# Performance work log

Measured on AMD Instinct MI355X. Metric: run time of the kernel, lower is better.

The kernel has to match this reference:

```python
import math
import jax, jax.numpy as jnp
import numpy as np

B, S, D = 4, 2048, 1024
EPS_LN = 1e-5
EPS_MAS = 1e-9


def layernorm(x, g, b):
    m = jnp.mean(x, axis=-1, keepdims=True)
    v = jnp.mean(jnp.square(x - m), axis=-1, keepdims=True)
    return (x - m) * jax.lax.rsqrt(v + EPS_LN) * g + b


def spl(x, proto_w, mu_w, mu_b, gate):
    # match_values = x @ proto^T / sqrt(d);  comp = silu(x @ mu^T + b)
    match = jnp.einsum('bsd,od->bso', x, proto_w) / math.sqrt(x.shape[-1])
    comp = jax.nn.silu(jnp.einsum('bsd,od->bso', x, mu_w) + mu_b)
    return comp, match, gate


def branch(comp, match, gate, passthrough):
    # mas_normalize on the 1-D gate vector (cost), broadcast over [B,S,D]
    cost = gate / (jnp.max(jnp.abs(gate)) + EPS_MAS)
    rl = match - cost
    mrl = jax.nn.relu(rl)
    mask = (rl > 0).astype(comp.dtype)
    return comp * mrl + passthrough * (1.0 - mask)


def causal_attention(q, k, v):
    # num_heads = 1, head_dim = D, is_causal=True
    scale = 1.0 / math.sqrt(q.shape[-1])
    scores = jnp.einsum('bqd,bkd->bqk', q, k) * scale
    causal = jnp.tril(jnp.ones((q.shape[1], k.shape[1]), dtype=bool))
    scores = jnp.where(causal, scores, jnp.asarray(-1e9, scores.dtype))
    p = jax.nn.softmax(scores, axis=-1)
    return jnp.einsum('bqk,bkd->bqd', p, v)


def setup_inputs() -> dict:
    key = jax.random.key(0)
    ks = jax.random.split(key, 16)
    d = D
    std = 0.02
    inp = {
        'x': jax.random.normal(ks[0], (B, S, d), jnp.float32),
        'ln_g': jnp.ones((d,), jnp.float32),
        'ln_b': jnp.zeros((d,), jnp.float32),
    }
    names = ['q', 'k', 'v', 'o']
    for i, n in enumerate(names):
        inp[f'{n}_mu_w'] = std * jax.random.normal(ks[1 + 3 * i], (d, d), jnp.float32)
        inp[f'{n}_mu_b'] = jnp.zeros((d,), jnp.float32)
        inp[f'{n}_proto'] = std * jax.random.normal(ks[2 + 3 * i], (d, d), jnp.float32)
        inp[f'{n}_gate'] = 0.1 * jax.random.normal(ks[3 + 3 * i], (d,), jnp.float32)
    return inp


def reference(x, ln_g, ln_b,
              q_mu_w, q_mu_b, q_proto, q_gate,
              k_mu_w, k_mu_b, k_proto, k_gate,
              v_mu_w, v_mu_b, v_proto, v_gate,
              o_mu_w, o_mu_b, o_proto, o_gate):
    ln1_out = layernorm(x, ln_g, ln_b)

    c_q, mv_q, g_q = spl(ln1_out, q_proto, q_mu_w, q_mu_b, q_gate)
    c_k, mv_k, g_k = spl(ln1_out, k_proto, k_mu_w, k_mu_b, k_gate)
    c_v, mv_v, g_v = spl(ln1_out, v_proto, v_mu_w, v_mu_b, v_gate)

    q = branch(c_q, mv_q, g_q, ln1_out)
    k = branch(c_k, mv_k, g_k, ln1_out)
    v = branch(c_v, mv_v, g_v, ln1_out)

    attn_out = causal_attention(q, k, v)

    c_o, mv_o, g_o = spl(attn_out, o_proto, o_mu_w, o_mu_b, o_gate)
    masked_o = branch(c_o, mv_o, g_o, attn_out)

    x_out = x + masked_o
    return x_out
```

## Files before the change

### kernel.cpp

```cpp
#include <hip/hip_runtime.h>
#include <hip/hip_bf16.h>
#include <cmath>
#include <cstdint>

typedef _Float16 f16;
typedef _Float16 f16x8 __attribute__((ext_vector_type(8)));
typedef float f32x4 __attribute__((ext_vector_type(4)));

#define D_ 1024
#define S_ 2048


__device__ __forceinline__ void gload_lds16(const void* g, void* l) {
  __builtin_amdgcn_global_load_lds(
      (const __attribute__((address_space(1))) void*)(unsigned long long)(uintptr_t)g,
      (__attribute__((address_space(3))) void*)(unsigned int)(uintptr_t)l,
      16, 0, 0);
}

__device__ __forceinline__ int lds_off(int row, int cb) {
  return (row << 5) + ((cb ^ ((row >> 1) & 3)) << 3);
}

__device__ __forceinline__ void split1024(float v, f16& h, f16& l) {
  float s = v * 1024.f;
  h = (f16)s;
  l = (f16)(s - (float)h);
}

#define MFMA16(a, b, c) __builtin_amdgcn_mfma_f32_16x16x32_f16((a), (b), (c), 0, 0, 0)

__global__ __launch_bounds__(256) void convert_w(
    const float* __restrict__ s0, const float* __restrict__ s1,
    const float* __restrict__ s2, const float* __restrict__ s3,
    const float* __restrict__ s4, const float* __restrict__ s5,
    const float* __restrict__ s6, const float* __restrict__ s7,
    f16* __restrict__ dst) {
  const float* srcs[8] = {s0, s1, s2, s3, s4, s5, s6, s7};
  const float* sp = srcs[blockIdx.y];
  f16* hi = dst + (size_t)blockIdx.y * 2097152;
  f16* lo = hi + 1048576;
  const int i = (blockIdx.x * 256 + threadIdx.x) << 2;
  float4 f = *(const float4*)(sp + i);
  __align__(8) f16 h4[4], l4[4];
  split1024(f.x, h4[0], l4[0]); split1024(f.y, h4[1], l4[1]);
  split1024(f.z, h4[2], l4[2]); split1024(f.w, h4[3], l4[3]);
  *(uint2*)(hi + i) = *(uint2*)h4;
  *(uint2*)(lo + i) = *(uint2*)l4;
}

__global__ __launch_bounds__(256) void cost_k(
    const float* __restrict__ g0, const float* __restrict__ g1,
    const float* __restrict__ g2, const float* __restrict__ g3,
    float* __restrict__ cost) {
  const float* gp = blockIdx.x == 0 ? g0 : blockIdx.x == 1 ? g1
                   : blockIdx.x == 2 ? g2 : g3;
  const int t = threadIdx.x;
  float4 v = *(const float4*)(gp + (t << 2));
  float mx = fmaxf(fmaxf(fabsf(v.x), fabsf(v.y)), fmaxf(fabsf(v.z), fabsf(v.w)));
  for (int o = 32; o; o >>= 1) mx = fmaxf(mx, __shfl_xor(mx, o, 64));
  __shared__ float red[4];
  if ((t & 63) == 0) red[t >> 6] = mx;
  __syncthreads();
  mx = fmaxf(fmaxf(red[0], red[1]), fmaxf(red[2], red[3]));
  const float den = mx + 1e-9f;
  float4 o = {v.x / den, v.y / den, v.z / den, v.w / den};
  *(float4*)(cost + (blockIdx.x << 10) + (t << 2)) = o;
}

__global__ __launch_bounds__(256) void layernorm_k(
    const float* __restrict__ x, const float* __restrict__ g,
    const float* __restrict__ bta, f16* __restrict__ Lh, f16* __restrict__ Ll) {
  const int row = blockIdx.x, t = threadIdx.x;
  const float* xr = x + (size_t)row * D_;
  float4 v = *(const float4*)(xr + (t << 2));
  float s = v.x + v.y + v.z + v.w;
  float q = v.x * v.x + v.y * v.y + v.z * v.z + v.w * v.w;
  for (int o = 32; o; o >>= 1) { s += __shfl_xor(s, o, 64); q += __shfl_xor(q, o, 64); }
  __shared__ float red[8];
  const int wid = t >> 6;
  if ((t & 63) == 0) { red[wid] = s; red[4 + wid] = q; }
  __syncthreads();
  s = red[0] + red[1] + red[2] + red[3];
  q = red[4] + red[5] + red[6] + red[7];
  const float mean = s * (1.f / D_);
  const float var = q * (1.f / D_) - mean * mean;
  const float inv = 1.f / sqrtf(var + 1e-5f);
  float4 gv = *(const float4*)(g + (t << 2));
  float4 bv = *(const float4*)(bta + (t << 2));
  __align__(8) f16 h4[4], l4[4];
  split1024((v.x - mean) * inv * gv.x + bv.x, h4[0], l4[0]);
  split1024((v.y - mean) * inv * gv.y + bv.y, h4[1], l4[1]);
  split1024((v.z - mean) * inv * gv.z + bv.z, h4[2], l4[2]);
  split1024((v.w - mean) * inv * gv.w + bv.w, h4[3], l4[3]);
  const size_t off = (size_t)row * D_ + (t << 2);
  *(uint2*)(Lh + off) = *(uint2*)h4;
  *(uint2*)(Ll + off) = *(uint2*)l4;
}

template <int EPI, int MUP>
__global__ __launch_bounds__(1024) void dual_gemm_v5(
    const f16* __restrict__ Ah, const f16* __restrict__ Al,
    const f16* __restrict__ Wph, const f16* __restrict__ Wpl,
    const f16* __restrict__ Wmh, const f16* __restrict__ Wml,
    const float* __restrict__ bias, const float* __restrict__ cost,
    const f16* __restrict__ passh, const f16* __restrict__ passl,
    const float* __restrict__ xres, f16* __restrict__ outh,
    f16* __restrict__ outl, float* __restrict__ outf) {
  __shared__ __align__(16) f16 smem[65536];
  const int tid = threadIdx.x, wid = tid >> 6, lane = tid & 63;
  const int row0 = blockIdx.x << 8, col0 = blockIdx.y << 7;
  const int wr = (wid & 3) << 6;
  const int wc = (wid >> 2) << 5;
  const int arow = lane & 15, cbk = lane >> 4;

  const int srow = tid >> 2;
  const int scA = ((tid & 3) ^ ((srow >> 1) & 3)) << 3;
  const int wrow = srow & 127;
  const int scW = ((tid & 3) ^ ((wrow >> 1) & 3)) << 3;
  const int wsel = tid >> 9;
  const int dstA = wid << 9;
  const int dstW = 16384 + (wid << 9);
  const int dstW2 = 24576 + (wid << 9);

  const f16* pAh = Ah + (size_t)(row0 + srow) * D_ + scA;
  const f16* pAl = Al + (size_t)(row0 + srow) * D_ + scA;
  const f16* pW1 = (wsel ? Wpl : Wph) + (size_t)(col0 + wrow) * D_ + scW;
  const f16* pW2 = (wsel ? Wml : Wmh) + (size_t)(col0 + wrow) * D_ + scW;

  const f32x4 zero = {0.f, 0.f, 0.f, 0.f};
  f32x4 accP[4][2], accM[4][2];
#pragma unroll
  for (int m = 0; m < 4; ++m)
#pragma unroll
    for (int n = 0; n < 2; ++n) { accP[m][n] = zero; accM[m][n] = zero; }

  int aoff[4], boff[2];
#pragma unroll
  for (int m = 0; m < 4; ++m) aoff[m] = lds_off(wr + m * 16 + arow, cbk);
#pragma unroll
  for (int n = 0; n < 2; ++n) boff[n] = lds_off(wc + n * 16 + arow, cbk);

  gload_lds16(pAh, smem + dstA);
  gload_lds16(pAl, smem + 8192 + dstA);
  gload_lds16(pW1, smem + dstW);
  gload_lds16(pW2, smem + dstW2);

  int cur = 0;
  for (int t = 0; t < 32; ++t) {
    const f16* bb = smem + (cur << 15);
    f16* nb = smem + ((cur ^ 1) << 15);
    const int kn = (t < 31) ? ((t + 1) << 5) : 0;

    gload_lds16(pAh + kn, nb + dstA);
    gload_lds16(pAl + kn, nb + 8192 + dstA);
    gload_lds16(pW1 + kn, nb + dstW);
    gload_lds16(pW2 + kn, nb + dstW2);
    asm volatile("s_waitcnt vmcnt(4)\n\ts_barrier" ::: "memory");
    __builtin_amdgcn_sched_barrier(0);

    f16x8 ah[4], al[4];
#pragma unroll
    for (int m = 0; m < 4; ++m) {
      ah[m] = *(const f16x8*)&bb[aoff[m]];
      al[m] = *(const f16x8*)&bb[8192 + aoff[m]];
    }
    __builtin_amdgcn_s_setprio(1);
#pragma unroll
    for (int n = 0; n < 2; ++n) {
      const f16x8 bph = *(const f16x8*)&bb[16384 + boff[n]];
      const f16x8 bpl = *(const f16x8*)&bb[20480 + boff[n]];
      const f16x8 bmh = *(const f16x8*)&bb[24576 + boff[n]];
      const f16x8 bml = *(const f16x8*)&bb[28672 + boff[n]];
#pragma unroll
      for (int m = 0; m < 4; ++m) {
        accP[m][n] = MFMA16(ah[m], bph, accP[m][n]);
        accP[m][n] = MFMA16(ah[m], bpl, accP[m][n]);
        accP[m][n] = MFMA16(al[m], bph, accP[m][n]);
        accM[m][n] = MFMA16(ah[m], bmh, accM[m][n]);
        accM[m][n] = MFMA16(ah[m], bml, accM[m][n]);
        if (MUP == 3) accM[m][n] = MFMA16(al[m], bmh, accM[m][n]);
      }
    }
    __builtin_amdgcn_s_setprio(0);
    asm volatile("s_waitcnt lgkmcnt(0)\n\ts_barrier" ::: "memory");
    cur ^= 1;
  }

#pragma unroll
  for (int m = 0; m < 4; ++m) {
    const int rb = row0 + wr + m * 16 + ((lane >> 4) << 2);
#pragma unroll
    for (int n = 0; n < 2; ++n) {
      const int col = col0 + wc + n * 16 + (lane & 15);
      const float cb2 = cost[col], bbv = bias[col];
#pragma unroll
      for (int j = 0; j < 4; ++j) {
        const size_t off = (size_t)(rb + j) * D_ + col;
        const float match = accP[m][n][j] * (1.f / 33554432.f);
        const float pre = accM[m][n][j] * (1.f / 1048576.f) + bbv;
        const float comp = pre / (1.f + expf(-pre));
        const float rl = match - cb2;
        float ov;
        if (rl > 0.f) ov = comp * rl;
        else ov = ((float)passh[off] + (float)passl[off]) * (1.f / 1024.f);
        if (EPI == 0) {
          f16 h, l; split1024(ov, h, l);
          outh[off] = h; outl[off] = l;
        } else {
          outf[off] = xres[off] + ov;
        }
      }
    }
  }
}

__global__ __launch_bounds__(256) void transpose_v(
    const f16* __restrict__ Vh, const f16* __restrict__ Vl,
    f16* __restrict__ VTh, f16* __restrict__ VTl) {
  const int iz = blockIdx.z, b = iz & 3;
  const f16* src = (iz >> 2) ? Vl : Vh;
  f16* dst = (iz >> 2) ? VTl : VTh;
  const int d0 = blockIdx.x << 6, s0 = blockIdx.y << 6;
  __shared__ f16 tl[64][65];
  const int c = threadIdx.x & 63, r4 = threadIdx.x >> 6;
  const f16* vb = src + (size_t)b * S_ * D_;
#pragma unroll
  for (int i = 0; i < 16; ++i) {
    const int sr = (r4 << 4) + i;
    tl[sr][c] = vb[(size_t)(s0 + sr) * D_ + d0 + c];
  }
  __syncthreads();
  f16* db = dst + (size_t)b * D_ * S_;
#pragma unroll
  for (int i = 0; i < 16; ++i) {
    const int dr = (r4 << 4) + i;
    db[(size_t)(d0 + dr) * S_ + s0 + c] = tl[c][dr];
  }
}

__global__ __launch_bounds__(512) void scores_v5(
    const f16* __restrict__ Qh, const f16* __restrict__ Ql,
    const f16* __restrict__ Kh, const f16* __restrict__ Kl,
    float* __restrict__ SC) {
  const int rt = blockIdx.x, ct = blockIdx.y, b = blockIdx.z;
  if (ct > rt) return;
  __shared__ __align__(16) f16 smem[32768];
  const int tid = threadIdx.x, wid = tid >> 6, lane = tid & 63;
  const int row0 = rt << 7, col0 = ct << 7;
  const int wr = (wid & 1) << 6;
  const int wc = (wid >> 1) << 5;
  const int arow = lane & 15, cbk = lane >> 4;

  const int srow = tid >> 2;
  const int sc4 = ((tid & 3) ^ ((srow >> 1) & 3)) << 3;
  const int dstb = wid << 9;

  const f16* pQh = Qh + ((size_t)b * S_ + row0 + srow) * D_ + sc4;
  const f16* pQl = Ql + ((size_t)b * S_ + row0 + srow) * D_ + sc4;
  const f16* pKh = Kh + ((size_t)b * S_ + col0 + srow) * D_ + sc4;
  const f16* pKl = Kl + ((size_t)b * S_ + col0 + srow) * D_ + sc4;

  const f32x4 zero = {0.f, 0.f, 0.f, 0.f};
  f32x4 acc[4][2];
#pragma unroll
  for (int m = 0; m < 4; ++m)
#pragma unroll
    for (int n = 0; n < 2; ++n) acc[m][n] = zero;

  int aoff[4], boff[2];
#pragma unroll
  for (int m = 0; m < 4; ++m) aoff[m] = lds_off(wr + m * 16 + arow, cbk);
#pragma unroll
  for (int n = 0; n < 2; ++n) boff[n] = lds_off(wc + n * 16 + arow, cbk);

  gload_lds16(pQh, smem + dstb);
  gload_lds16(pQl, smem + 4096 + dstb);
  gload_lds16(pKh, smem + 8192 + dstb);
  gload_lds16(pKl, smem + 12288 + dstb);

  int cur = 0;
  for (int t = 0; t < 32; ++t) {
    const f16* bb = smem + (cur << 14);
    f16* nb = smem + ((cur ^ 1) << 14);
    const int kn = (t < 31) ? ((t + 1) << 5) : 0;

    gload_lds16(pQh + kn, nb + dstb);
    gload_lds16(pQl + kn, nb + 4096 + dstb);
    gload_lds16(pKh + kn, nb + 8192 + dstb);
    gload_lds16(pKl + kn, nb + 12288 + dstb);
    asm volatile("s_waitcnt vmcnt(4)\n\ts_barrier" ::: "memory");
    __builtin_amdgcn_sched_barrier(0);

    f16x8 ah[4], al[4];
#pragma unroll
    for (int m = 0; m < 4; ++m) {
      ah[m] = *(const f16x8*)&bb[aoff[m]];
      al[m] = *(const f16x8*)&bb[4096 + aoff[m]];
    }
    __builtin_amdgcn_s_setprio(1);
#pragma unroll
    for (int n = 0; n < 2; ++n) {
      const f16x8 bh = *(const f16x8*)&bb[8192 + boff[n]];
      const f16x8 bl = *(const f16x8*)&bb[12288 + boff[n]];
#pragma unroll
      for (int m = 0; m < 4; ++m) {
        acc[m][n] = MFMA16(ah[m], bh, acc[m][n]);
        acc[m][n] = MFMA16(ah[m], bl, acc[m][n]);
        acc[m][n] = MFMA16(al[m], bh, acc[m][n]);
      }
    }
    __builtin_amdgcn_s_setprio(0);
    asm volatile("s_waitcnt lgkmcnt(0)\n\ts_barrier" ::: "memory");
    cur ^= 1;
  }

  float* scb = SC + (size_t)b * S_ * S_;
#pragma unroll
  for (int m = 0; m < 4; ++m) {
    const int rb = row0 + wr + m * 16 + ((lane >> 4) << 2);
#pragma unroll
    for (int n = 0; n < 2; ++n) {
      const int col = col0 + wc + n * 16 + (lane & 15);
#pragma unroll
      for (int j = 0; j < 4; ++j)
        scb[(size_t)(rb + j) * S_ + col] = acc[m][n][j] * (1.f / 33554432.f);
    }
  }
}

__global__ __launch_bounds__(256) void softmax_rows(float* __restrict__ SC) {
  const int r = blockIdx.x;
  const int s = r & 2047;
  float* rowf = SC + (size_t)r * S_;
  const int t = threadIdx.x, c0 = t << 3;
  float f[8];
  float4 u0 = *(const float4*)(rowf + c0);
  float4 u1 = *(const float4*)(rowf + c0 + 4);
  f[0] = u0.x; f[1] = u0.y; f[2] = u0.z; f[3] = u0.w;
  f[4] = u1.x; f[5] = u1.y; f[6] = u1.z; f[7] = u1.w;
  float mx = -3.0e38f;
#pragma unroll
  for (int j = 0; j < 8; ++j)
    if (c0 + j <= s) mx = fmaxf(mx, f[j]);
  for (int o = 32; o; o >>= 1) mx = fmaxf(mx, __shfl_xor(mx, o, 64));
  __shared__ float red[8];
  const int wid = t >> 6;
  if ((t & 63) == 0) red[wid] = mx;
  __syncthreads();
  mx = fmaxf(fmaxf(red[0], red[1]), fmaxf(red[2], red[3]));
  float e[8];
  float sum = 0.f;
#pragma unroll
  for (int j = 0; j < 8; ++j) {
    e[j] = (c0 + j <= s) ? expf(f[j] - mx) : 0.f;
    sum += e[j];
  }
  for (int o = 32; o; o >>= 1) sum += __shfl_xor(sum, o, 64);
  if ((t & 63) == 0) red[4 + wid] = sum;
  __syncthreads();
  sum = red[4] + red[5] + red[6] + red[7];
  f16* rowh = (f16*)rowf;
  __align__(16) f16 ph[8], pl[8];
#pragma unroll
  for (int j = 0; j < 8; ++j) {
    float p = (e[j] / sum) * 2048.f;
    ph[j] = (f16)p;
    pl[j] = (f16)(p - (float)ph[j]);
  }
  *(uint4*)(rowh + c0) = *(uint4*)ph;
  *(uint4*)(rowh + 2048 + c0) = *(uint4*)pl;
}

__global__ __launch_bounds__(512) void pv_v5(
    const f16* __restrict__ P, const f16* __restrict__ VTh,
    const f16* __restrict__ VTl, f16* __restrict__ Ath, f16* __restrict__ Atl) {
  const int rt = blockIdx.x, ct = blockIdx.y, b = blockIdx.z;
  __shared__ __align__(16) f16 smem[32768];
  const int tid = threadIdx.x, wid = tid >> 6, lane = tid & 63;
  const int row0 = rt << 7, col0 = ct << 7;
  const int wr = (wid & 1) << 6;
  const int wc = (wid >> 1) << 5;
  const int arow = lane & 15, cbk = lane >> 4;

  const int srow = tid >> 2;
  const int sc4 = ((tid & 3) ^ ((srow >> 1) & 3)) << 3;
  const int dstb = wid << 9;

  const f16* pPh = P + ((size_t)b * S_ + row0 + srow) * 4096 + sc4;
  const f16* pPl = pPh + 2048;
  const f16* pVh = VTh + (size_t)b * D_ * S_ + (size_t)(col0 + srow) * S_ + sc4;
  const f16* pVl = VTl + (size_t)b * D_ * S_ + (size_t)(col0 + srow) * S_ + sc4;

  const f32x4 zero = {0.f, 0.f, 0.f, 0.f};
  f32x4 acc[4][2];
#pragma unroll
  for (int m = 0; m < 4; ++m)
#pragma unroll
    for (int n = 0; n < 2; ++n) acc[m][n] = zero;

  int aoff[4], boff[2];
#pragma unroll
  for (int m = 0; m < 4; ++m) aoff[m] = lds_off(wr + m * 16 + arow, cbk);
#pragma unroll
  for (int n = 0; n < 2; ++n) boff[n] = lds_off(wc + n * 16 + arow, cbk);

  const int steps = (rt + 1) << 2;

  gload_lds16(pPh, smem + dstb);
  gload_lds16(pPl, smem + 4096 + dstb);
  gload_lds16(pVh, smem + 8192 + dstb);
  gload_lds16(pVl, smem + 12288 + dstb);

  int cur = 0;
  for (int t = 0; t < steps; ++t) {
    const f16* bb = smem + (cur << 14);
    f16* nb = smem + ((cur ^ 1) << 14);
    const int kn = (t < steps - 1) ? ((t + 1) << 5) : 0;

    gload_lds16(pPh + kn, nb + dstb);
    gload_lds16(pPl + kn, nb + 4096 + dstb);
    gload_lds16(pVh + kn, nb + 8192 + dstb);
    gload_lds16(pVl + kn, nb + 12288 + dstb);
    asm volatile("s_waitcnt vmcnt(4)\n\ts_barrier" ::: "memory");
    __builtin_amdgcn_sched_barrier(0);

    f16x8 ah[4], al[4];
#pragma unroll
    for (int m = 0; m < 4; ++m) {
      ah[m] = *(const f16x8*)&bb[aoff[m]];
      al[m] = *(const f16x8*)&bb[4096 + aoff[m]];
    }
    __builtin_amdgcn_s_setprio(1);
#pragma unroll
    for (int n = 0; n < 2; ++n) {
      const f16x8 bh = *(const f16x8*)&bb[8192 + boff[n]];
      const f16x8 bl = *(const f16x8*)&bb[12288 + boff[n]];
#pragma unroll
      for (int m = 0; m < 4; ++m) {
        acc[m][n] = MFMA16(ah[m], bh, acc[m][n]);
        acc[m][n] = MFMA16(ah[m], bl, acc[m][n]);
        acc[m][n] = MFMA16(al[m], bh, acc[m][n]);
      }
    }
    __builtin_amdgcn_s_setprio(0);
    asm volatile("s_waitcnt lgkmcnt(0)\n\ts_barrier" ::: "memory");
    cur ^= 1;
  }

#pragma unroll
  for (int m = 0; m < 4; ++m) {
    const int rb = row0 + wr + m * 16 + ((lane >> 4) << 2);
#pragma unroll
    for (int n = 0; n < 2; ++n) {
      const int col = col0 + wc + n * 16 + (lane & 15);
#pragma unroll
      for (int j = 0; j < 4; ++j) {
        const float at = acc[m][n][j] * (1.f / 2097152.f);
        const size_t off = ((size_t)b * S_ + rb + j) * D_ + col;
        f16 h, l; split1024(at, h, l);
        Ath[off] = h; Atl[off] = l;
      }
    }
  }
}

extern "C" void kernel_launch(void* const* d_in, const int* in_sizes, int n_in,
                              void* d_out, int out_size, void* d_ws, size_t ws_size,
                              hipStream_t stream) {
  (void)in_sizes; (void)n_in; (void)out_size; (void)ws_size;
  const float* x      = (const float*)d_in[0];
  const float* ln_g   = (const float*)d_in[1];
  const float* ln_b   = (const float*)d_in[2];
  const float* q_mu_w = (const float*)d_in[3];
  const float* q_mu_b = (const float*)d_in[4];
  const float* q_pro  = (const float*)d_in[5];
  const float* q_gate = (const float*)d_in[6];
  const float* k_mu_w = (const float*)d_in[7];
  const float* k_mu_b = (const float*)d_in[8];
  const float* k_pro  = (const float*)d_in[9];
  const float* k_gate = (const float*)d_in[10];
  const float* v_mu_w = (const float*)d_in[11];
  const float* v_mu_b = (const float*)d_in[12];
  const float* v_pro  = (const float*)d_in[13];
  const float* v_gate = (const float*)d_in[14];
  const float* o_mu_w = (const float*)d_in[15];
  const float* o_mu_b = (const float*)d_in[16];
  const float* o_pro  = (const float*)d_in[17];
  const float* o_gate = (const float*)d_in[18];

  char* w = (char*)d_ws;
  f16* WB = (f16*)w;
  const size_t WS = 2097152;
  f16* Lh  = (f16*)(w + 33554432);
  f16* Ll  = (f16*)(w + 50331648);
  f16* Qh  = (f16*)(w + 67108864);
  f16* Ql  = (f16*)(w + 83886080);
  f16* Kh  = (f16*)(w + 100663296);
  f16* Kl  = (f16*)(w + 117440512);
  f16* VTh = (f16*)(w + 134217728);
  f16* VTl = (f16*)(w + 150994944);
  float* SC = (float*)(w + 167772160);
  float* COST = (float*)(w + 234881024);
  f16* Vh = (f16*)SC;
  f16* Vl = (f16*)(w + 184549376);
  f16* Ath = Qh;  f16* Atl = Ql;

  convert_w<<<dim3(1024, 8), 256, 0, stream>>>(
      q_pro, q_mu_w, k_pro, k_mu_w, v_pro, v_mu_w, o_pro, o_mu_w, WB);
  cost_k<<<4, 256, 0, stream>>>(q_gate, k_gate, v_gate, o_gate, COST);
  layernorm_k<<<8192, 256, 0, stream>>>(x, ln_g, ln_b, Lh, Ll);

  dual_gemm_v5<0, 3><<<dim3(32, 8), 1024, 0, stream>>>(
      Lh, Ll, WB, WB + 1048576, WB + WS, WB + WS + 1048576,
      q_mu_b, COST, Lh, Ll, nullptr, Qh, Ql, nullptr);
  dual_gemm_v5<0, 3><<<dim3(32, 8), 1024, 0, stream>>>(
      Lh, Ll, WB + 2 * WS, WB + 2 * WS + 1048576, WB + 3 * WS, WB + 3 * WS + 1048576,
      k_mu_b, COST + 1024, Lh, Ll, nullptr, Kh, Kl, nullptr);
  dual_gemm_v5<0, 3><<<dim3(32, 8), 1024, 0, stream>>>(
      Lh, Ll, WB + 4 * WS, WB + 4 * WS + 1048576, WB + 5 * WS, WB + 5 * WS + 1048576,
      v_mu_b, COST + 2048, Lh, Ll, nullptr, Vh, Vl, nullptr);

  transpose_v<<<dim3(16, 32, 8), 256, 0, stream>>>(Vh, Vl, VTh, VTl);
  scores_v5<<<dim3(16, 16, 4), 512, 0, stream>>>(Qh, Ql, Kh, Kl, SC);
  softmax_rows<<<8192, 256, 0, stream>>>(SC);
  pv_v5<<<dim3(16, 8, 4), 512, 0, stream>>>((const f16*)SC, VTh, VTl, Ath, Atl);

  dual_gemm_v5<1, 2><<<dim3(32, 8), 1024, 0, stream>>>(
      Ath, Atl, WB + 6 * WS, WB + 6 * WS + 1048576, WB + 7 * WS, WB + 7 * WS + 1048576,
      o_mu_b, COST + 3072, Ath, Atl, x, nullptr, nullptr, (float*)d_out);
}
```

Measured before the change: 696.5 us.

## Shrink dual GEMM tiles to 128x64 with 256-thread single-buffered blocks

The dual projection GEMM moves from 256x128 tiles with 1024-thread blocks and double-buffered 128KB LDS to 128x64 tiles with 256-thread blocks, single-buffered 32KB LDS and a launch bound allowing 4 blocks per CU. This gives 1024 blocks instead of 256, so the 256 CUs of the device get more work and better load balance. The trade-off is no overlap of global loads with MFMA inside a block, since each step waits with vmcnt(0). It also means more redundant global traffic from the smaller tiles, and latency hiding now depends on other resident blocks. An unused stage_tile helper is also added.

```diff
diff --git a/kernel.cpp b/kernel.cpp
--- a/kernel.cpp
+++ b/kernel.cpp
@@ -29,6 +29,15 @@
 }
 
 #define MFMA16(a, b, c) __builtin_amdgcn_mfma_f32_16x16x32_f16((a), (b), (c), 0, 0, 0)
+
+__device__ __forceinline__ void stage_tile(const f16* __restrict__ src, int ld,
+                                           f16* lds, int wid, int lane) {
+  const int r = (wid << 5) + (lane >> 2);
+  const int c = (lane & 3) ^ ((r >> 1) & 3);
+  const f16* g0 = src + (size_t)r * ld + (c << 3);
+  gload_lds16(g0, lds + (wid << 10));
+  gload_lds16(g0 + (size_t)(ld << 4), lds + (wid << 10) + 512);
+}
 
 __global__ __launch_bounds__(256) void convert_w(
     const float* __restrict__ s0, const float* __restrict__ s1,
@@ -99,7 +108,7 @@
 }
 
 template <int EPI, int MUP>
-__global__ __launch_bounds__(1024) void dual_gemm_v5(
+__global__ __launch_bounds__(256, 4) void dual_gemm_v6(
     const f16* __restrict__ Ah, const f16* __restrict__ Al,
     const f16* __restrict__ Wph, const f16* __restrict__ Wpl,
     const f16* __restrict__ Wmh, const f16* __restrict__ Wml,
@@ -107,26 +116,24 @@
     const f16* __restrict__ passh, const f16* __restrict__ passl,
     const float* __restrict__ xres, f16* __restrict__ outh,
     f16* __restrict__ outl, float* __restrict__ outf) {
-  __shared__ __align__(16) f16 smem[65536];
+  __shared__ __align__(16) f16 smem[16384];
   const int tid = threadIdx.x, wid = tid >> 6, lane = tid & 63;
-  const int row0 = blockIdx.x << 8, col0 = blockIdx.y << 7;
-  const int wr = (wid & 3) << 6;
-  const int wc = (wid >> 2) << 5;
+  const int row0 = blockIdx.x << 7, col0 = blockIdx.y << 6;
+  const int wr = (wid & 1) << 6, wc = (wid >> 1) << 5;
   const int arow = lane & 15, cbk = lane >> 4;
 
-  const int srow = tid >> 2;
-  const int scA = ((tid & 3) ^ ((srow >> 1) & 3)) << 3;
-  const int wrow = srow & 127;
-  const int scW = ((tid & 3) ^ ((wrow >> 1) & 3)) << 3;
-  const int wsel = tid >> 9;
-  const int dstA = wid << 9;
-  const int dstW = 16384 + (wid << 9);
-  const int dstW2 = 24576 + (wid << 9);
-
-  const f16* pAh = Ah + (size_t)(row0 + srow) * D_ + scA;
-  const f16* pAl = Al + (size_t)(row0 + srow) * D_ + scA;
-  const f16* pW1 = (wsel ? Wpl : Wph) + (size_t)(col0 + wrow) * D_ + scW;
-  const f16* pW2 = (wsel ? Wml : Wmh) + (size_t)(col0 + wrow) * D_ + scW;
+  const int sr = tid >> 2;
+  const int sc = ((tid & 3) ^ ((sr >> 1) & 3)) << 3;
+  const int dstw = wid << 9;
+
+  const f16* pA0 = Ah + (size_t)(row0 + sr) * D_ + sc;
+  const f16* pA1 = Ah + (size_t)(row0 + 64 + sr) * D_ + sc;
+  const f16* pL0 = Al + (size_t)(row0 + sr) * D_ + sc;
+  const f16* pL1 = Al + (size_t)(row0 + 64 + sr) * D_ + sc;
+  const f16* pPh = Wph + (size_t)(col0 + sr) * D_ + sc;
+  const f16* pPl = Wpl + (size_t)(col0 + sr) * D_ + sc;
+  const f16* pMh = Wmh + (size_t)(col0 + sr) * D_ + sc;
+  const f16* pMl = Wml + (size_t)(col0 + sr) * D_ + sc;
 
   const f32x4 zero = {0.f, 0.f, 0.f, 0.f};
   f32x4 accP[4][2], accM[4][2];
@@ -141,37 +148,32 @@
 #pragma unroll
   for (int n = 0; n < 2; ++n) boff[n] = lds_off(wc + n * 16 + arow, cbk);
 
-  gload_lds16(pAh, smem + dstA);
-  gload_lds16(pAl, smem + 8192 + dstA);
-  gload_lds16(pW1, smem + dstW);
-  gload_lds16(pW2, smem + dstW2);
-
-  int cur = 0;
   for (int t = 0; t < 32; ++t) {
-    const f16* bb = smem + (cur << 15);
-    f16* nb = smem + ((cur ^ 1) << 15);
-    const int kn = (t < 31) ? ((t + 1) << 5) : 0;
-
-    gload_lds16(pAh + kn, nb + dstA);
-    gload_lds16(pAl + kn, nb + 8192 + dstA);
-    gload_lds16(pW1 + kn, nb + dstW);
-    gload_lds16(pW2 + kn, nb + dstW2);
-    asm volatile("s_waitcnt vmcnt(4)\n\ts_barrier" ::: "memory");
+    const int k = t << 5;
+    gload_lds16(pA0 + k, smem + dstw);
+    gload_lds16(pA1 + k, smem + 2048 + dstw);
+    gload_lds16(pL0 + k, smem + 4096 + dstw);
+    gload_lds16(pL1 + k, smem + 6144 + dstw);
+    gload_lds16(pPh + k, smem + 8192 + dstw);
+    gload_lds16(pPl + k, smem + 10240 + dstw);
+    gload_lds16(pMh + k, smem + 12288 + dstw);
+    gload_lds16(pMl + k, smem + 14336 + dstw);
+    asm volatile("s_waitcnt vmcnt(0)\n\ts_barrier" ::: "memory");
     __builtin_amdgcn_sched_barrier(0);
 
     f16x8 ah[4], al[4];
 #pragma unroll
     for (int m = 0; m < 4; ++m) {
-      ah[m] = *(const f16x8*)&bb[aoff[m]];
-      al[m] = *(const f16x8*)&bb[8192 + aoff[m]];
+      ah[m] = *(const f16x8*)&smem[aoff[m]];
+      al[m] = *(const f16x8*)&smem[4096 + aoff[m]];
     }
     __builtin_amdgcn_s_setprio(1);
 #pragma unroll
     for (int n = 0; n < 2; ++n) {
-      const f16x8 bph = *(const f16x8*)&bb[16384 + boff[n]];
-      const f16x8 bpl = *(const f16x8*)&bb[20480 + boff[n]];
-      const f16x8 bmh = *(const f16x8*)&bb[24576 + boff[n]];
-      const f16x8 bml = *(const f16x8*)&bb[28672 + boff[n]];
+      const f16x8 bph = *(const f16x8*)&smem[8192 + boff[n]];
+      const f16x8 bpl = *(const f16x8*)&smem[10240 + boff[n]];
+      const f16x8 bmh = *(const f16x8*)&smem[12288 + boff[n]];
+      const f16x8 bml = *(const f16x8*)&smem[14336 + boff[n]];
 #pragma unroll
       for (int m = 0; m < 4; ++m) {
         accP[m][n] = MFMA16(ah[m], bph, accP[m][n]);
@@ -184,7 +186,6 @@
     }
     __builtin_amdgcn_s_setprio(0);
     asm volatile("s_waitcnt lgkmcnt(0)\n\ts_barrier" ::: "memory");
-    cur ^= 1;
   }
 
 #pragma unroll
@@ -511,13 +512,13 @@
   cost_k<<<4, 256, 0, stream>>>(q_gate, k_gate, v_gate, o_gate, COST);
   layernorm_k<<<8192, 256, 0, stream>>>(x, ln_g, ln_b, Lh, Ll);
 
-  dual_gemm_v5<0, 3><<<dim3(32, 8), 1024, 0, stream>>>(
+  dual_gemm_v6<0, 3><<<dim3(64, 16), 256, 0, stream>>>(
       Lh, Ll, WB, WB + 1048576, WB + WS, WB + WS + 1048576,
       q_mu_b, COST, Lh, Ll, nullptr, Qh, Ql, nullptr);
-  dual_gemm_v5<0, 3><<<dim3(32, 8), 1024, 0, stream>>>(
+  dual_gemm_v6<0, 3><<<dim3(64, 16), 256, 0, stream>>>(
       Lh, Ll, WB + 2 * WS, WB + 2 * WS + 1048576, WB + 3 * WS, WB + 3 * WS + 1048576,
       k_mu_b, COST + 1024, Lh, Ll, nullptr, Kh, Kl, nullptr);
-  dual_gemm_v5<0, 3><<<dim3(32, 8), 1024, 0, stream>>>(
+  dual_gemm_v6<0, 3><<<dim3(64, 16), 256, 0, stream>>>(
       Lh, Ll, WB + 4 * WS, WB + 4 * WS + 1048576, WB + 5 * WS, WB + 5 * WS + 1048576,
       v_mu_b, COST + 2048, Lh, Ll, nullptr, Vh, Vl, nullptr);
 
@@ -526,7 +527,7 @@
   softmax_rows<<<8192, 256, 0, stream>>>(SC);
   pv_v5<<<dim3(16, 8, 4), 512, 0, stream>>>((const f16*)SC, VTh, VTl, Ath, Atl);
 
-  dual_gemm_v5<1, 2><<<dim3(32, 8), 1024, 0, stream>>>(
+  dual_gemm_v6<1, 2><<<dim3(64, 16), 256, 0, stream>>>(
       Ath, Atl, WB + 6 * WS, WB + 6 * WS + 1048576, WB + 7 * WS, WB + 7 * WS + 1048576,
       o_mu_b, COST + 3072, Ath, Atl, x, nullptr, nullptr, (float*)d_out);
 }
```

New measurement: 734.8 us. 5.5% more time.
